# Kernel tuning notes

Measured on AMD Instinct MI355X. Metric: run time of the kernel, lower is better.

Reference implementation:

```python
import jax, jax.numpy as jnp
import numpy as np

BN_EPS = 1e-5
NEG_SLOPE = 0.2


def setup_inputs() -> dict:
    key = jax.random.key(0)
    ks = jax.random.split(key, 3)
    B, C, N, O = 8, 64, 4096, 64
    x = jax.random.normal(ks[0], (B, C, N), dtype=jnp.float32)
    W = jax.random.normal(ks[1], (O, 2 * C), dtype=jnp.float32) * 0.05
    gamma = jnp.ones((O,), dtype=jnp.float32)
    beta = jnp.zeros((O,), dtype=jnp.float32)
    run_mean = jnp.zeros((O,), dtype=jnp.float32)
    run_var = jnp.ones((O,), dtype=jnp.float32)
    return {"x": x, "W": W, "gamma": gamma, "beta": beta,
            "run_mean": run_mean, "run_var": run_var, "k": 20}


def _edgeconv(x, W, gamma, beta, run_mean, run_var, k):
    # x: [B, C, N] -> features [B, N, C]
    xt = jnp.transpose(x, (0, 2, 1))                      # [B, N, C]
    # pairwise_distance = -||xi||^2 + 2 xi.xj - ||xj||^2 (negative sq dist)
    sq = jnp.sum(xt * xt, axis=2, keepdims=True)          # [B, N, 1]
    inner = jnp.einsum('bnc,bmc->bnm', xt, xt)            # [B, N, N]
    pd = 2.0 * inner - sq - jnp.transpose(sq, (0, 2, 1))  # [B, N, N]
    _, idx = jax.lax.top_k(pd, k)                         # [B, N, k] nearest (incl. self)
    # gather neighbor features per batch
    neighbors = jax.vmap(lambda f, i: f[i])(xt, idx)      # [B, N, k, C]
    x_exp = xt[:, :, None, :]                             # [B, N, 1, C]
    edge = jnp.concatenate(
        [jnp.broadcast_to(x_exp, neighbors.shape), neighbors - x_exp], axis=3)  # [B,N,k,2C]
    # 1x1 conv == matmul over channel dim
    y = jnp.einsum('bnkc,oc->bnko', edge, W)              # [B, N, k, O]
    scale = gamma / jnp.sqrt(run_var + BN_EPS)
    y = y * scale + (beta - run_mean * scale)
    y = jnp.where(y >= 0, y, NEG_SLOPE * y)               # LeakyReLU(0.2)
    out = jnp.max(y, axis=2)                              # [B, N, O] max over k
    return jnp.transpose(out, (0, 2, 1))                  # [B, O, N]


def reference(x, W, gamma, beta, run_mean, run_var, k):
    return _edgeconv(x, W, gamma, beta, run_mean, run_var, k)
```

## Files before the change

kernel.cpp:

```cpp
#include <hip/hip_runtime.h>

#define B 8
#define C 64
#define N 4096
#define O 64
#define KNN 20
#define PQ 4
#define BN_EPS 1e-5f
#define NEG_SLOPE 0.2f

typedef _Float16 f16x8 __attribute__((ext_vector_type(8)));
typedef float    f32x4 __attribute__((ext_vector_type(4)));
#define MFMA16(a, b, c) __builtin_amdgcn_mfma_f32_16x16x32_f16(a, b, c, 0, 0, 0)

__device__ __forceinline__ void sorted_insert(float (&d)[KNN], int (&id)[KNN],
                                              float r, int m) {
    bool c[KNN];
    #pragma unroll
    for (int j = 0; j < KNN; ++j) c[j] = d[j] < r;
    #pragma unroll
    for (int j = 0; j < KNN - 1; ++j) {
        d[j]  = __builtin_amdgcn_fmed3f(d[j], d[j + 1], r);
        id[j] = c[j + 1] ? id[j + 1] : (c[j] ? m : id[j]);
    }
    d[KNN - 1]  = c[KNN - 1] ? r : d[KNN - 1];
    id[KNN - 1] = c[KNN - 1] ? m : id[KNN - 1];
}

__global__ __launch_bounds__(256) void k_transpose(const float* __restrict__ x,
                                                   float* __restrict__ Xt,
                                                   float* __restrict__ sq,
                                                   char* __restrict__ AHL) {
    __shared__ float lds[C][65];
    int b    = blockIdx.x >> 6;
    int n0   = (blockIdx.x & 63) << 6;
    int lane = threadIdx.x & 63;
    int w    = threadIdx.x >> 6;
    #pragma unroll
    for (int i = 0; i < 16; ++i) {
        int c = w * 16 + i;
        lds[c][lane] = x[(size_t)b * C * N + (size_t)c * N + n0 + lane];
    }
    __syncthreads();
    #pragma unroll
    for (int i = 0; i < 16; ++i) {
        int nl = w * 16 + i;
        Xt[(size_t)b * N * C + (size_t)(n0 + nl) * C + lane] = lds[lane][nl];
    }
    {
        int n_loc = threadIdx.x >> 2;
        int cg    = threadIdx.x & 3;
        float s = 0.f;
        #pragma unroll
        for (int ii = 0; ii < 16; ++ii) {
            float v = lds[cg * 16 + ii][n_loc];
            s = fmaf(v, v, s);
        }
        s += __shfl_xor(s, 1, 64);
        s += __shfl_xor(s, 2, 64);
        if (cg == 0) sq[b * N + n0 + n_loc] = s;
    }
    int s2  = threadIdx.x & 15;
    int rem = threadIdx.x >> 4;
    int qd  = rem & 3;
    int hh  = (rem >> 2) & 1;
    int tt  = rem >> 3;
    int kb  = hh * 32 + qd * 8;
    for (int i = 0; i < 4; ++i) {
        int rowl = i * 16 + s2;
        f16x8 pk;
        #pragma unroll
        for (int ii = 0; ii < 8; ++ii) {
            float v = lds[kb + ii][rowl];
            _Float16 hv = (_Float16)v;
            if (tt) hv = (_Float16)(v - (float)hv);
            pk[ii] = hv;
        }
        char* dst = AHL + ((size_t)b << 20) + (size_t)((n0 >> 4) + i) * 4096
                  + tt * 2048 + hh * 1024 + qd * 256 + s2 * 16;
        *(f16x8*)dst = pk;
    }
}

__global__ __launch_bounds__(256, 2) void k_ab(const float* __restrict__ Xt,
                                               const float* __restrict__ W,
                                               float* __restrict__ av,
                                               float* __restrict__ bv) {
    int b  = blockIdx.x >> 5;
    int n0 = (blockIdx.x & 31) << 7;
    int o  = threadIdx.x & 63;
    int w  = __builtin_amdgcn_readfirstlane((int)(threadIdx.x >> 6));
    float wa[C], wb[C];
    #pragma unroll
    for (int c = 0; c < C; ++c) {
        float w1 = W[o * 2 * C + c];
        float w2 = W[o * 2 * C + C + c];
        wa[c] = w1 - w2;
        wb[c] = w2;
    }
    const float* xb = Xt + (size_t)b * N * C;
    for (int i = 0; i < 32; ++i) {
        int n = n0 + w * 32 + i;
        const float4* xr4 = (const float4*)(xb + (size_t)n * C);
        float aa = 0.f, bb = 0.f;
        #pragma unroll
        for (int c4 = 0; c4 < C / 4; ++c4) {
            float4 xv = xr4[c4];
            aa = fmaf(xv.x, wa[c4 * 4 + 0], aa);
            bb = fmaf(xv.x, wb[c4 * 4 + 0], bb);
            aa = fmaf(xv.y, wa[c4 * 4 + 1], aa);
            bb = fmaf(xv.y, wb[c4 * 4 + 1], bb);
            aa = fmaf(xv.z, wa[c4 * 4 + 2], aa);
            bb = fmaf(xv.z, wb[c4 * 4 + 2], bb);
            aa = fmaf(xv.w, wa[c4 * 4 + 3], aa);
            bb = fmaf(xv.w, wb[c4 * 4 + 3], bb);
        }
        size_t oidx = ((size_t)b * N + n) * O + o;
        av[oidx] = aa;
        bv[oidx] = bb;
    }
}

__global__ __launch_bounds__(256, 3) void k_knn(const char* __restrict__ AHL,
                                                const float* __restrict__ sq,
                                                float* __restrict__ pdg,
                                                int* __restrict__ pig) {
    int bid  = blockIdx.x;
    int rb   = bid >> 4;
    int b    = (bid >> 1) & 7;
    int h    = bid & 1;
    int tid  = threadIdx.x;
    int lane = tid & 63;
    int w    = __builtin_amdgcn_readfirstlane(tid >> 6);
    int quad = lane >> 4;
    const char*  AHLb = AHL + ((size_t)b << 20);
    const float* sqb  = sq + b * N;
    int cbase0 = h * (N / 2);
    const char* Asrc = AHLb + (size_t)cbase0 * 256;

    const char* qb = AHLb + (size_t)(rb * 4 + w) * 4096 + lane * 16;
    f16x8 bh0 = *(const f16x8*)(qb);
    f16x8 bh1 = *(const f16x8*)(qb + 1024);
    f16x8 bl0 = *(const f16x8*)(qb + 2048);
    f16x8 bl1 = *(const f16x8*)(qb + 3072);

    float d[KNN]; int id[KNN];
    float pv[PQ]; int pi[PQ]; int pc = 0;
    #pragma unroll
    for (int j = 0; j < PQ; ++j) { pv[j] = 0.f; pi[j] = 0; }

    const char* p0 = Asrc + lane * 16;
    f16x8 na0 = *(const f16x8*)(p0);
    f16x8 na1 = *(const f16x8*)(p0 + 1024);
    f16x8 na2 = *(const f16x8*)(p0 + 2048);
    f16x8 na3 = *(const f16x8*)(p0 + 3072);
    float4 nsq = *(const float4*)(sqb + cbase0 + quad * 4);

    #pragma unroll
    for (int it = 0; it < 5; ++it) {
        f16x8 a0 = na0, a1 = na1, a2 = na2, a3 = na3;
        float4 sqv = nsq;
        {
            const char* p = Asrc + (size_t)(it + 1) * 4096 + lane * 16;
            na0 = *(const f16x8*)(p);
            na1 = *(const f16x8*)(p + 1024);
            na2 = *(const f16x8*)(p + 2048);
            na3 = *(const f16x8*)(p + 3072);
            nsq = *(const float4*)(sqb + cbase0 + (it + 1) * 16 + quad * 4);
        }
        f32x4 acc = {0.f, 0.f, 0.f, 0.f};
        acc = MFMA16(a0, bh0, acc);
        acc = MFMA16(a1, bh1, acc);
        acc = MFMA16(a0, bl0, acc);
        acc = MFMA16(a1, bl1, acc);
        acc = MFMA16(a2, bh0, acc);
        acc = MFMA16(a3, bh1, acc);
        int c0 = cbase0 + it * 16 + quad * 4;
        #pragma unroll
        for (int r = 0; r < 4; ++r) {
            float sc = fmaf(2.f, acc[r],
                            -((r == 0) ? sqv.x : (r == 1) ? sqv.y
                                       : (r == 2) ? sqv.z : sqv.w));
            d[it * 4 + r]  = sc;
            id[it * 4 + r] = c0 + r;
        }
    }
    #pragma unroll
    for (int i = 0; i < KNN - 1; ++i) {
        #pragma unroll
        for (int j = 0; j < KNN - 1 - i; ++j) {
            bool sw = d[j] > d[j + 1];
            float tv = d[j]; int ti = id[j];
            d[j]      = sw ? d[j + 1] : d[j];
            id[j]     = sw ? id[j + 1] : id[j];
            d[j + 1]  = sw ? tv : d[j + 1];
            id[j + 1] = sw ? ti : id[j + 1];
        }
    }
    float thr = d[0];
    thr = fmaxf(thr, __shfl_xor(thr, 16, 64));
    thr = fmaxf(thr, __shfl_xor(thr, 32, 64));

    #pragma unroll 1
    for (int it = 5; it < 128; ++it) {
        f16x8 a0 = na0, a1 = na1, a2 = na2, a3 = na3;
        float4 sqv = nsq;
        if (it + 1 < 128) {
            const char* p = Asrc + (size_t)(it + 1) * 4096 + lane * 16;
            na0 = *(const f16x8*)(p);
            na1 = *(const f16x8*)(p + 1024);
            na2 = *(const f16x8*)(p + 2048);
            na3 = *(const f16x8*)(p + 3072);
            nsq = *(const float4*)(sqb + cbase0 + (it + 1) * 16 + quad * 4);
        }
        f32x4 acc = {0.f, 0.f, 0.f, 0.f};
        acc = MFMA16(a0, bh0, acc);
        acc = MFMA16(a1, bh1, acc);
        acc = MFMA16(a0, bl0, acc);
        acc = MFMA16(a1, bl1, acc);
        acc = MFMA16(a2, bh0, acc);
        acc = MFMA16(a3, bh1, acc);
        int c0 = cbase0 + it * 16 + quad * 4;
        #pragma unroll
        for (int r = 0; r < 4; ++r) {
            float sc = fmaf(2.f, acc[r],
                            -((r == 0) ? sqv.x : (r == 1) ? sqv.y
                                       : (r == 2) ? sqv.z : sqv.w));
            if (sc > thr) {
                #pragma unroll
                for (int j = 0; j < PQ; ++j) {
                    bool sel = (pc == j);
                    pv[j] = sel ? sc : pv[j];
                    pi[j] = sel ? (c0 + r) : pi[j];
                }
                ++pc;
            }
            if (__any(pc == PQ)) {
                #pragma unroll
                for (int j = 0; j < PQ; ++j)
                    if (j < pc && pv[j] > d[0]) sorted_insert(d, id, pv[j], pi[j]);
                pc = 0;
                float t = d[0];
                t = fmaxf(t, __shfl_xor(t, 16, 64));
                t = fmaxf(t, __shfl_xor(t, 32, 64));
                thr = fmaxf(thr, t);
            }
        }
    }
    #pragma unroll
    for (int j = 0; j < PQ; ++j)
        if (j < pc && pv[j] > d[0]) sorted_insert(d, id, pv[j], pi[j]);

    #pragma unroll 1
    for (int step = 0; step < 2; ++step) {
        int off = (step == 0) ? 32 : 16;
        bool active = (step == 0) ? (quad < 2) : (quad == 0);
        for (int j = KNN - 1; j >= 0; --j) {
            float rv = __shfl(d[j], lane + off, 64);
            int   ri = __shfl(id[j], lane + off, 64);
            bool ins = active && (rv > d[0]);
            if (!__any(ins)) break;
            if (ins) sorted_insert(d, id, rv, ri);
        }
    }
    if (lane < 16) {
        size_t rr = (size_t)b * N + rb * 64 + w * 16 + lane;
        float* po = pdg + (rr * 2 + h) * KNN;
        int*   qo = pig + (rr * 2 + h) * KNN;
        #pragma unroll
        for (int j = 0; j < KNN; ++j) { po[j] = d[j]; qo[j] = id[j]; }
    }
}

__global__ __launch_bounds__(128) void k_merge(const float* __restrict__ pdg,
                                               const int* __restrict__ pig,
                                               int* __restrict__ knn) {
    __shared__ float sd[128][41];
    __shared__ int   si[128][41];
    int t = threadIdx.x;
    size_t rr = (size_t)blockIdx.x * 128 + t;
    const float* pr = pdg + rr * (2 * KNN);
    const int*   qr = pig + rr * (2 * KNN);
    #pragma unroll
    for (int j = 0; j < 2 * KNN; ++j) { sd[t][j] = pr[j]; si[t][j] = qr[j]; }
    int i = KNN - 1, j = KNN - 1;
    int* op = knn + rr * KNN;
    for (int o = 0; o < KNN; ++o) {
        bool t0 = (j < 0) || (i >= 0 && sd[t][i] >= sd[t][KNN + j]);
        op[o] = t0 ? si[t][i] : si[t][KNN + j];
        if (t0) --i; else --j;
    }
}

__global__ __launch_bounds__(256) void k_out(const float* __restrict__ av,
                                             const float* __restrict__ bv,
                                             const int* __restrict__ knn,
                                             const float* __restrict__ gamma,
                                             const float* __restrict__ beta,
                                             const float* __restrict__ rmean,
                                             const float* __restrict__ rvar,
                                             float* __restrict__ out) {
    __shared__ float lds[64][65];
    int b    = blockIdx.x >> 6;
    int n0   = (blockIdx.x & 63) << 6;
    int lane = threadIdx.x & 63;
    int w    = __builtin_amdgcn_readfirstlane((int)(threadIdx.x >> 6));
    int o    = lane;
    float scale = gamma[o] * rsqrtf(rvar[o] + BN_EPS);
    float bias  = fmaf(-rmean[o], scale, beta[o]);
    const float* bvb = bv + (size_t)b * N * O;
    for (int i = 0; i < 16; ++i) {
        int n = n0 + w * 16 + i;
        const int* kn = knn + ((size_t)b * N + n) * KNN;
        float mx = -3.4e38f, mn = 3.4e38f;
        #pragma unroll
        for (int j = 0; j < KNN; ++j) {
            float v = bvb[(size_t)kn[j] * O + o];
            mx = fmaxf(mx, v);
            mn = fminf(mn, v);
        }
        float a   = av[((size_t)b * N + n) * O + o];
        float sel = (scale >= 0.f) ? (a + mx) : (a + mn);
        float y   = fmaf(sel, scale, bias);
        y = fmaxf(y, NEG_SLOPE * y);
        lds[o][w * 16 + i] = y;
    }
    __syncthreads();
    int r  = threadIdx.x >> 2;
    int c0 = (threadIdx.x & 3) << 4;
    float* ob = out + (size_t)b * O * N + (size_t)r * N + n0;
    #pragma unroll
    for (int j = 0; j < 16; j += 4) {
        float4 v;
        v.x = lds[r][c0 + j + 0];
        v.y = lds[r][c0 + j + 1];
        v.z = lds[r][c0 + j + 2];
        v.w = lds[r][c0 + j + 3];
        *(float4*)(ob + c0 + j) = v;
    }
}

extern "C" void kernel_launch(void* const* d_in, const int* in_sizes, int n_in,
                              void* d_out, int out_size, void* d_ws, size_t ws_size,
                              hipStream_t stream) {
    const float* x     = (const float*)d_in[0];
    const float* W     = (const float*)d_in[1];
    const float* gamma = (const float*)d_in[2];
    const float* beta  = (const float*)d_in[3];
    const float* rmean = (const float*)d_in[4];
    const float* rvar  = (const float*)d_in[5];
    float* out = (float*)d_out;

    char* wsb = (char*)d_ws;
    float* Xt  = (float*)(wsb);
    float* sqn = (float*)(wsb + 8388608);
    float* av  = (float*)(wsb + 8519680);
    float* bvv = (float*)(wsb + 16908288);
    int*   knn = (int*)  (wsb + 25296896);
    char*  AHL =         (wsb + 27918336);
    float* pdg = (float*)(wsb + 36306944);
    int*   pig = (int*)  (wsb + 41549824);

    k_transpose<<<512, 256, 0, stream>>>(x, Xt, sqn, AHL);
    k_ab<<<256, 256, 0, stream>>>(Xt, W, av, bvv);
    k_knn<<<1024, 256, 0, stream>>>(AHL, sqn, pdg, pig);
    k_merge<<<256, 128, 0, stream>>>(pdg, pig, knn);
    k_out<<<512, 256, 0, stream>>>(av, bvv, knn, gamma, beta, rmean, rvar, out);
}
```

Baseline: 380.2 us.

## Triple-buffer candidate tile prefetch in kNN loop and interleave batches across blocks

Replaces the single-stage register prefetch in the kNN scan with a three-deep rotating buffer, unrolled three iterations per loop trip, so global loads for a tile are issued three iterations ahead of their MFMA use. Occupancy hint drops from 3 to 2 blocks per CU to make room for the extra registers. Block-to-(batch, tile) mapping in k_ab, k_knn and k_out is changed so consecutive blocks cover different batches, altering cache and memory-channel locality. The trade is lower occupancy and more register pressure in exchange for longer latency hiding.

```diff
diff --git a/kernel.cpp b/kernel.cpp
--- a/kernel.cpp
+++ b/kernel.cpp
@@ -86,8 +86,8 @@
                                                const float* __restrict__ W,
                                                float* __restrict__ av,
                                                float* __restrict__ bv) {
-    int b  = blockIdx.x >> 5;
-    int n0 = (blockIdx.x & 31) << 7;
+    int b  = blockIdx.x & 7;
+    int n0 = ((blockIdx.x >> 3) & 31) << 7;
     int o  = threadIdx.x & 63;
     int w  = __builtin_amdgcn_readfirstlane((int)(threadIdx.x >> 6));
     float wa[C], wb[C];
@@ -121,14 +121,62 @@
     }
 }
 
-__global__ __launch_bounds__(256, 3) void k_knn(const char* __restrict__ AHL,
+#define KBODY(A0, A1, A2, A3, SQ4, ITV)                                      \
+  {                                                                          \
+    const int it_ = (ITV);                                                   \
+    f32x4 acc = {0.f, 0.f, 0.f, 0.f};                                        \
+    acc = MFMA16(A0, bh0, acc);                                              \
+    acc = MFMA16(A1, bh1, acc);                                              \
+    acc = MFMA16(A0, bl0, acc);                                              \
+    acc = MFMA16(A1, bl1, acc);                                              \
+    acc = MFMA16(A2, bh0, acc);                                              \
+    acc = MFMA16(A3, bh1, acc);                                              \
+    float4 sql = SQ4;                                                        \
+    {                     \
+        int itn = (it_ + 3 < 127) ? (it_ + 3) : 127;                         \
+        const char* p = Asrc + (size_t)itn * 4096 + lane * 16;               \
+        A0 = *(const f16x8*)(p);                                             \
+        A1 = *(const f16x8*)(p + 1024);                                      \
+        A2 = *(const f16x8*)(p + 2048);                                      \
+        A3 = *(const f16x8*)(p + 3072);                                      \
+        SQ4 = *(const float4*)(sqb + cbase0 + itn * 16 + quad * 4);          \
+    }                                                                        \
+    int c0 = cbase0 + it_ * 16 + quad * 4;                                   \
+    _Pragma("unroll")                                                        \
+    for (int r = 0; r < 4; ++r) {                                            \
+        float sc = fmaf(2.f, acc[r],                                         \
+                        -((r == 0) ? sql.x : (r == 1) ? sql.y                \
+                                   : (r == 2) ? sql.z : sql.w));             \
+        if (sc > thr) {                                                      \
+            _Pragma("unroll")                                                \
+            for (int j = 0; j < PQ; ++j) {                                   \
+                bool sel = (pc == j);                                        \
+                pv[j] = sel ? sc : pv[j];                                    \
+                pi[j] = sel ? (c0 + r) : pi[j];                              \
+            }                                                                \
+            ++pc;                                                            \
+        }                                                                    \
+        if (__any(pc == PQ)) {                                               \
+            _Pragma("unroll")                                                \
+            for (int j = 0; j < PQ; ++j)                                     \
+                if (j < pc && pv[j] > d[0]) sorted_insert(d, id, pv[j], pi[j]); \
+            pc = 0;                                                          \
+            float t = d[0];                                                  \
+            t = fmaxf(t, __shfl_xor(t, 16, 64));                             \
+            t = fmaxf(t, __shfl_xor(t, 32, 64));                             \
+            thr = fmaxf(thr, t);                                             \
+        }                                                                    \
+    }                                                                        \
+  }
+
+__global__ __launch_bounds__(256, 2) void k_knn(const char* __restrict__ AHL,
                                                 const float* __restrict__ sq,
                                                 float* __restrict__ pdg,
                                                 int* __restrict__ pig) {
     int bid  = blockIdx.x;
     int rb   = bid >> 4;
-    int b    = (bid >> 1) & 7;
-    int h    = bid & 1;
+    int b    = bid & 7;
+    int h    = (bid >> 3) & 1;
     int tid  = threadIdx.x;
     int lane = tid & 63;
     int w    = __builtin_amdgcn_readfirstlane(tid >> 6);
@@ -201,51 +249,32 @@
     thr = fmaxf(thr, __shfl_xor(thr, 16, 64));
     thr = fmaxf(thr, __shfl_xor(thr, 32, 64));
 
+    f16x8 xa0 = na0, xa1 = na1, xa2 = na2, xa3 = na3; float4 xsq = nsq;
+    f16x8 ya0, ya1, ya2, ya3; float4 ysq;
+    f16x8 za0, za1, za2, za3; float4 zsq;
+    {
+        const char* p = Asrc + (size_t)6 * 4096 + lane * 16;
+        ya0 = *(const f16x8*)(p);
+        ya1 = *(const f16x8*)(p + 1024);
+        ya2 = *(const f16x8*)(p + 2048);
+        ya3 = *(const f16x8*)(p + 3072);
+        ysq = *(const float4*)(sqb + cbase0 + 6 * 16 + quad * 4);
+    }
+    {
+        const char* p = Asrc + (size_t)7 * 4096 + lane * 16;
+        za0 = *(const f16x8*)(p);
+        za1 = *(const f16x8*)(p + 1024);
+        za2 = *(const f16x8*)(p + 2048);
+        za3 = *(const f16x8*)(p + 3072);
+        zsq = *(const float4*)(sqb + cbase0 + 7 * 16 + quad * 4);
+    }
+
     #pragma unroll 1
-    for (int it = 5; it < 128; ++it) {
-        f16x8 a0 = na0, a1 = na1, a2 = na2, a3 = na3;
-        float4 sqv = nsq;
-        if (it + 1 < 128) {
-            const char* p = Asrc + (size_t)(it + 1) * 4096 + lane * 16;
-            na0 = *(const f16x8*)(p);
-            na1 = *(const f16x8*)(p + 1024);
-            na2 = *(const f16x8*)(p + 2048);
-            na3 = *(const f16x8*)(p + 3072);
-            nsq = *(const float4*)(sqb + cbase0 + (it + 1) * 16 + quad * 4);
-        }
-        f32x4 acc = {0.f, 0.f, 0.f, 0.f};
-        acc = MFMA16(a0, bh0, acc);
-        acc = MFMA16(a1, bh1, acc);
-        acc = MFMA16(a0, bl0, acc);
-        acc = MFMA16(a1, bl1, acc);
-        acc = MFMA16(a2, bh0, acc);
-        acc = MFMA16(a3, bh1, acc);
-        int c0 = cbase0 + it * 16 + quad * 4;
-        #pragma unroll
-        for (int r = 0; r < 4; ++r) {
-            float sc = fmaf(2.f, acc[r],
-                            -((r == 0) ? sqv.x : (r == 1) ? sqv.y
-                                       : (r == 2) ? sqv.z : sqv.w));
-            if (sc > thr) {
-                #pragma unroll
-                for (int j = 0; j < PQ; ++j) {
-                    bool sel = (pc == j);
-                    pv[j] = sel ? sc : pv[j];
-                    pi[j] = sel ? (c0 + r) : pi[j];
-                }
-                ++pc;
-            }
-            if (__any(pc == PQ)) {
-                #pragma unroll
-                for (int j = 0; j < PQ; ++j)
-                    if (j < pc && pv[j] > d[0]) sorted_insert(d, id, pv[j], pi[j]);
-                pc = 0;
-                float t = d[0];
-                t = fmaxf(t, __shfl_xor(t, 16, 64));
-                t = fmaxf(t, __shfl_xor(t, 32, 64));
-                thr = fmaxf(thr, t);
-            }
-        }
+    for (int g = 0; g < 41; ++g) {
+        int itb = 5 + g * 3;
+        KBODY(xa0, xa1, xa2, xa3, xsq, itb);
+        KBODY(ya0, ya1, ya2, ya3, ysq, itb + 1);
+        KBODY(za0, za1, za2, za3, zsq, itb + 2);
     }
     #pragma unroll
     for (int j = 0; j < PQ; ++j)
@@ -301,8 +330,8 @@
                                              const float* __restrict__ rvar,
                                              float* __restrict__ out) {
     __shared__ float lds[64][65];
-    int b    = blockIdx.x >> 6;
-    int n0   = (blockIdx.x & 63) << 6;
+    int b    = blockIdx.x & 7;
+    int n0   = (blockIdx.x >> 3) << 6;
     int lane = threadIdx.x & 63;
     int w    = __builtin_amdgcn_readfirstlane((int)(threadIdx.x >> 6));
     int o    = lane;
```

After: 379.6 us. Within noise of the previous version (-0.1%).
